# Kernel optimization log

Hardware: AMD Instinct MI355X
Metric: run time of the kernel (lower is better)

Reference implementation:

```python
import jax, jax.numpy as jnp
import numpy as np

T, BS, NH, DS, HD, R = 1024, 4, 16, 32, 128, 8
D_INNER = NH * HD

def setup_inputs() -> dict:
    key = jax.random.key(0)
    k1, k2, k3, k4, k5 = jax.random.split(key, 5)
    return {
        "B_proj": jax.random.normal(k1, (T, BS, NH, DS, R), jnp.float32),
        "X_proj": jax.random.normal(k2, (T, BS, NH, HD, R), jnp.float32),
        "alpha_raw": jax.random.normal(k3, (T, BS, NH), jnp.float32),
        "alpha_bias": jnp.full((NH,), 2.2, jnp.float32) + 0.01 * jax.random.normal(k4, (NH,), jnp.float32),
        "z": jax.random.normal(k5, (T, BS, D_INNER), jnp.float32),
        "H0": jnp.zeros((BS, NH, DS, HD), jnp.float32),
    }

def _elman_scan(B_proj, X_proj, alpha_raw, alpha_bias, z, H0):
    # alpha in (0, 0.5): sigmoid(-softplus(.))
    alpha_all = jax.nn.sigmoid(-jax.nn.softplus(alpha_raw + alpha_bias))  # [T,B,NH]

    def step(H, inp):
        B_t, X_t, a_t, z_t = inp
        # rank-R MIMO update: [B,NH,DS,HD]
        update = jnp.einsum('bhnr,bhpr->bhnp', B_t, X_t)
        H_new = jax.nn.silu(a_t[:, :, None, None] * H + update)
        y_t = H_new.sum(axis=2).reshape(H.shape[0], -1)  # [B, d_inner]
        out_t = y_t * jax.nn.silu(z_t + y_t)
        return H_new, out_t

    H_final, output = jax.lax.scan(step, H0, (B_proj, X_proj, alpha_all, z))
    return output, H_final

def reference(B_proj, X_proj, alpha_raw, alpha_bias, z, H0):
    return _elman_scan(B_proj, X_proj, alpha_raw, alpha_bias, z, H0)
```

## Files before the change

kernel.cpp:

```cpp
#include <hip/hip_runtime.h>


namespace {
constexpr int T  = 1024;
constexpr int BS = 4;
constexpr int NH = 16;
constexpr int DS = 32;
constexpr int HD = 128;
constexpr int R  = 8;
constexpr int DI = NH * HD;
constexpr int GROUP = 4;

constexpr unsigned BF_T  = BS * NH * DS * R;
constexpr unsigned XF_T  = BS * NH * HD * R;
constexpr unsigned A_T   = BS * NH;
constexpr unsigned OUT_T = BS * DI;

constexpr int SPAN   = 64;
constexpr int WARM   = 24;
constexpr int NSLICE = 16;

constexpr float LOG2E = 1.4426950408889634f;

typedef __attribute__((ext_vector_type(8)))  _Float16 half8;
typedef __attribute__((ext_vector_type(16))) float    f32x16;
typedef __attribute__((ext_vector_type(4)))  unsigned u32x4;

__device__ __forceinline__ float fast_exp(float x) {
    return __builtin_amdgcn_exp2f(x * LOG2E);
}
__device__ __forceinline__ float fast_silu(float x) {
    return x * __builtin_amdgcn_rcpf(1.0f + __builtin_amdgcn_exp2f(x * -LOG2E));
}

__global__ __launch_bounds__(256)
void alpha_kernel(const float* __restrict__ ar_, const float* __restrict__ ab_,
                  float* __restrict__ alpha_) {
    int i = blockIdx.x * 256 + threadIdx.x;
    float v = ar_[i] + ab_[i & (NH - 1)];
    alpha_[i] = __builtin_amdgcn_rcpf(2.0f + fast_exp(v));
}

template<bool PRE>
__global__ __launch_bounds__(256, 2)
void elman32_kernel(const float* __restrict__ B_,
                    const float* __restrict__ X_,
                    const float* __restrict__ a_,
                    const float* __restrict__ ab_,
                    const float* __restrict__ z_,
                    const float* __restrict__ H0_,
                    float* __restrict__ out_,
                    float* __restrict__ Hf_)
{
    const int lane  = threadIdx.x & 63;
    const int W     = blockIdx.x * 4 + (threadIdx.x >> 6);
    const int slice = W >> 8;
    const int Wl    = W & 255;
    const int pc    = Wl & 3;
    const int bh    = Wl >> 2;
    const int h     = bh & (NH - 1);
    const int b     = bh >> 4;
    const int l31   = lane & 31;
    const int khalf = lane >> 5;
    const int p0    = pc * 32;

    const int t_begin   = slice * SPAN - (slice ? WARM : 0);
    const int ngroups   = (slice ? (SPAN + WARM) : SPAN) / GROUP;
    const int emit_from = slice ? (WARM / GROUP) : 0;

    const unsigned mz = khalf ? 0u : 0xFFFFFFFFu;
    const float abv = PRE ? 0.0f : ab_[h];

    f32x16 H;
    if (slice == 0) {
        #pragma unroll
        for (int i = 0; i < 16; ++i) {
            int row = (i & 3) + 8 * (i >> 2) + 4 * khalf;
            H[i] = H0_[(unsigned)bh * 4096u + (unsigned)row * 128u
                       + (unsigned)(p0 + l31)];
        }
    } else {
        #pragma unroll
        for (int i = 0; i < 16; ++i) H[i] = 0.0f;
    }

    unsigned oB = (unsigned)bh * (DS * R) + (unsigned)l31 * R
                + (unsigned)t_begin * BF_T;
    unsigned oX = (unsigned)bh * (HD * R) + (unsigned)(p0 + l31) * R
                + (unsigned)t_begin * XF_T;
    unsigned oA = (unsigned)bh + (unsigned)(t_begin + (lane & 3)) * A_T;
    unsigned oZ = (unsigned)b * DI + (unsigned)h * HD + (unsigned)(p0 + l31)
                + (unsigned)t_begin * OUT_T;
    unsigned oO = oZ;

    u32x4 afr[GROUP], bfr[GROUP];
    float zr[GROUP];
    float av;

    auto pk8 = [](const float4& v0, const float4& v1) -> u32x4 {
        u32x4 u;
        u.x = __builtin_bit_cast(unsigned, __builtin_amdgcn_cvt_pkrtz(v0.x, v0.y));
        u.y = __builtin_bit_cast(unsigned, __builtin_amdgcn_cvt_pkrtz(v0.z, v0.w));
        u.z = __builtin_bit_cast(unsigned, __builtin_amdgcn_cvt_pkrtz(v1.x, v1.y));
        u.w = __builtin_bit_cast(unsigned, __builtin_amdgcn_cvt_pkrtz(v1.z, v1.w));
        return u;
    };

    auto refill = [&](int s) {
        float4 b0 = *(const float4*)(B_ + oB + (unsigned)s * BF_T);
        float4 b1 = *(const float4*)(B_ + oB + (unsigned)s * BF_T + 4u);
        float4 x0 = *(const float4*)(X_ + oX + (unsigned)s * XF_T);
        float4 x1 = *(const float4*)(X_ + oX + (unsigned)s * XF_T + 4u);
        u32x4 a = pk8(b0, b1);
        a.x &= mz; a.y &= mz; a.z &= mz; a.w &= mz;
        afr[s] = a;
        bfr[s] = pk8(x0, x1);
        zr[s]  = z_[oZ + (unsigned)s * OUT_T];
    };

    #pragma unroll
    for (int s = 0; s < GROUP; ++s) refill(s);
    av = a_[oA];
    oB += GROUP * BF_T; oX += GROUP * XF_T;
    oZ += GROUP * OUT_T; oA += GROUP * A_T;

    auto step = [&](int s, bool emit) {
        float ar = __int_as_float(
            __builtin_amdgcn_readlane(__float_as_int(av), s));
        float alpha = PRE ? ar
                          : __builtin_amdgcn_rcpf(2.0f + fast_exp(ar + abv));
        f32x16 c;
        #pragma unroll
        for (int i = 0; i < 16; ++i) c[i] = alpha * H[i];
        f32x16 d = __builtin_amdgcn_mfma_f32_32x32x16_f16(
            __builtin_bit_cast(half8, afr[s]),
            __builtin_bit_cast(half8, bfr[s]), c, 0, 0, 0);
        #pragma unroll
        for (int i = 0; i < 16; ++i) H[i] = fast_silu(d[i]);
        float yp = 0.0f;
        #pragma unroll
        for (int i = 0; i < 16; ++i) yp += H[i];
        float y2 = yp + __shfl_xor(yp, 32, 64);
        float gt = y2 * fast_silu(zr[s] + y2);
        if (emit && lane < 32) out_[oO + (unsigned)s * OUT_T] = gt;
    };

    #pragma unroll 1
    for (int g = 0; g < ngroups - 1; ++g) {
        const bool emit = g >= emit_from;
        #pragma unroll
        for (int s = 0; s < GROUP; ++s) {
            step(s, emit);
            refill(s);
        }
        av = a_[oA];
        oB += GROUP * BF_T; oX += GROUP * XF_T;
        oZ += GROUP * OUT_T; oA += GROUP * A_T;
        oO += GROUP * OUT_T;
    }
    #pragma unroll
    for (int s = 0; s < GROUP; ++s) step(s, true);

    if (slice == NSLICE - 1) {
        #pragma unroll
        for (int i = 0; i < 16; ++i) {
            int row = (i & 3) + 8 * (i >> 2) + 4 * khalf;
            Hf_[(unsigned)bh * 4096u + (unsigned)row * 128u
                + (unsigned)(p0 + l31)] = H[i];
        }
    }
}
}

extern "C" void kernel_launch(void* const* d_in, const int* in_sizes, int n_in,
                              void* d_out, int out_size, void* d_ws, size_t ws_size,
                              hipStream_t stream) {
    const float* B_proj     = (const float*)d_in[0];
    const float* X_proj     = (const float*)d_in[1];
    const float* alpha_raw  = (const float*)d_in[2];
    const float* alpha_bias = (const float*)d_in[3];
    const float* z          = (const float*)d_in[4];
    const float* H0         = (const float*)d_in[5];

    float* out = (float*)d_out;
    float* Hf  = out + (size_t)T * BS * DI;

    const size_t alpha_bytes = (size_t)T * BS * NH * sizeof(float);
    if (ws_size >= alpha_bytes) {
        float* aw = (float*)d_ws;
        alpha_kernel<<<T * BS * NH / 256, 256, 0, stream>>>(alpha_raw, alpha_bias, aw);
        elman32_kernel<true><<<1024, 256, 0, stream>>>(
            B_proj, X_proj, aw, alpha_bias, z, H0, out, Hf);
    } else {
        elman32_kernel<false><<<1024, 256, 0, stream>>>(
            B_proj, X_proj, alpha_raw, alpha_bias, z, H0, out, Hf);
    }
}
```

Baseline: 123.2 us.

## Shorten warmup, double-buffer alpha loads, and tree-reduce the row sum

Cuts the per-slice warmup from 24 to 16 steps, so each non-first slice runs fewer redundant recurrence steps. The alpha load is now issued two groups ahead (av0/av1 ping-pong) to hide its latency across a whole group. The serial 16-term sum becomes a pairwise tree to shorten the dependency chain. The shorter warmup relies on alpha < 0.5 decaying the initial state quickly enough, which trades some accuracy risk for less work.

```diff
diff --git a/kernel.cpp b/kernel.cpp
--- a/kernel.cpp
+++ b/kernel.cpp
@@ -17,7 +17,7 @@
 constexpr unsigned OUT_T = BS * DI;
 
 constexpr int SPAN   = 64;
-constexpr int WARM   = 24;
+constexpr int WARM   = 16;
 constexpr int NSLICE = 16;
 
 constexpr float LOG2E = 1.4426950408889634f;
@@ -95,7 +95,7 @@
 
     u32x4 afr[GROUP], bfr[GROUP];
     float zr[GROUP];
-    float av;
+    float av0, av1;
 
     auto pk8 = [](const float4& v0, const float4& v1) -> u32x4 {
         u32x4 u;
@@ -120,11 +120,12 @@
 
     #pragma unroll
     for (int s = 0; s < GROUP; ++s) refill(s);
-    av = a_[oA];
-    oB += GROUP * BF_T; oX += GROUP * XF_T;
-    oZ += GROUP * OUT_T; oA += GROUP * A_T;
-
-    auto step = [&](int s, bool emit) {
+    av0 = a_[oA];
+    av1 = a_[oA + (unsigned)GROUP * A_T];
+    oA += 2u * GROUP * A_T;
+    oB += GROUP * BF_T; oX += GROUP * XF_T; oZ += GROUP * OUT_T;
+
+    auto step = [&](int s, bool emit, float av) {
         float ar = __int_as_float(
             __builtin_amdgcn_readlane(__float_as_int(av), s));
         float alpha = PRE ? ar
@@ -137,29 +138,43 @@
             __builtin_bit_cast(half8, bfr[s]), c, 0, 0, 0);
         #pragma unroll
         for (int i = 0; i < 16; ++i) H[i] = fast_silu(d[i]);
-        float yp = 0.0f;
-        #pragma unroll
-        for (int i = 0; i < 16; ++i) yp += H[i];
+        float t0 = H[0] + H[1],   t1 = H[2] + H[3];
+        float t2 = H[4] + H[5],   t3 = H[6] + H[7];
+        float t4 = H[8] + H[9],   t5 = H[10] + H[11];
+        float t6 = H[12] + H[13], t7 = H[14] + H[15];
+        t0 += t1; t2 += t3; t4 += t5; t6 += t7;
+        t0 += t2; t4 += t6;
+        float yp = t0 + t4;
         float y2 = yp + __shfl_xor(yp, 32, 64);
         float gt = y2 * fast_silu(zr[s] + y2);
         if (emit && lane < 32) out_[oO + (unsigned)s * OUT_T] = gt;
     };
 
-    #pragma unroll 1
-    for (int g = 0; g < ngroups - 1; ++g) {
-        const bool emit = g >= emit_from;
+    auto group_body = [&](bool emit, float av) {
         #pragma unroll
         for (int s = 0; s < GROUP; ++s) {
-            step(s, emit);
+            step(s, emit, av);
             refill(s);
         }
-        av = a_[oA];
         oB += GROUP * BF_T; oX += GROUP * XF_T;
-        oZ += GROUP * OUT_T; oA += GROUP * A_T;
-        oO += GROUP * OUT_T;
-    }
+        oZ += GROUP * OUT_T; oO += GROUP * OUT_T;
+    };
+
+    const int P = (ngroups - 2) / 2;
+    int g = 0;
+    #pragma unroll 1
+    for (int gg = 0; gg < P; ++gg) {
+        group_body(g >= emit_from, av0);
+        av0 = a_[oA];
+        ++g;
+        group_body(g >= emit_from, av1);
+        av1 = a_[oA + (unsigned)GROUP * A_T];
+        oA += 2u * GROUP * A_T;
+        ++g;
+    }
+    group_body(true, av0);
     #pragma unroll
-    for (int s = 0; s < GROUP; ++s) step(s, true);
+    for (int s = 0; s < GROUP; ++s) step(s, true, av1);
 
     if (slice == NSLICE - 1) {
         #pragma unroll
```

Measured after the change: 112.9 us. 8.4% less time.
